# Performance work log

Measured on AMD Instinct MI355X. Metric: run time of the kernel, lower is better.

Reference implementation:

```python
import jax, jax.numpy as jnp
import numpy as np

D_MODEL = 256
NUM_WAVES = 8192
NUM_TRANSITIONS = 8192
NUM_TARGETS = 4096
BATCH = 4
TOP_K = 3


def setup_inputs() -> dict:
    key = jax.random.key(0)
    ks = jax.random.split(key, 16)
    d = D_MODEL
    inp = {
        'wave': jax.random.normal(ks[0], (BATCH, NUM_WAVES, d), jnp.float32),
        'transition': jax.random.normal(ks[1], (BATCH, NUM_TRANSITIONS, d), jnp.float32),
        'target': jax.random.normal(ks[2], (BATCH, NUM_TARGETS, d), jnp.float32),
        # learned adjacency logits (init: randn * 0.1)
        'w2t_adj': jax.random.normal(ks[3], (NUM_WAVES, NUM_TRANSITIONS), jnp.float32) * 0.1,
        't2t_adj': jax.random.normal(ks[4], (NUM_TRANSITIONS, NUM_TARGETS), jnp.float32) * 0.1,
        'temperature': jnp.array(1.0, jnp.float32),
        # gumbel noise (fixed sample, as drawn inside F.gumbel_softmax)
        'g_wt': jax.random.gumbel(ks[5], (NUM_WAVES, NUM_TRANSITIONS), jnp.float32),
        'g_tt': jax.random.gumbel(ks[6], (NUM_TRANSITIONS, NUM_TARGETS), jnp.float32),
        # wave->transition edge-weight predictor MLP: Linear(2d,d) ReLU Linear(d,1) Sigmoid
        'wt_w1': jax.random.normal(ks[7], (2 * d, d), jnp.float32) / np.sqrt(2 * d),
        'wt_b1': jnp.zeros((d,), jnp.float32),
        'wt_w2': jax.random.normal(ks[8], (d, 1), jnp.float32) / np.sqrt(d),
        'wt_b2': jnp.zeros((1,), jnp.float32),
        # transition->target predictor MLP
        'tt_w1': jax.random.normal(ks[9], (2 * d, d), jnp.float32) / np.sqrt(2 * d),
        'tt_b1': jnp.zeros((d,), jnp.float32),
        'tt_w2': jax.random.normal(ks[10], (d, 1), jnp.float32) / np.sqrt(d),
        'tt_b2': jnp.zeros((1,), jnp.float32),
    }
    return inp


def _gumbel_softmax(logits, gumbel_noise, tau):
    return jax.nn.softmax((logits + gumbel_noise) / tau, axis=-1)


def _generate_edges(probs, src_feat, tgt_feat, w1, b1, w2, b2):
    # probs: [S, T]; src_feat: [B, S, d]; tgt_feat: [B, T, d]
    S = probs.shape[0]
    top_vals, top_idx = jax.lax.top_k(probs, TOP_K)  # [S, k]
    src_idx = jnp.broadcast_to(jnp.arange(S)[:, None], (S, TOP_K)).reshape(-1)  # [S*k]
    tgt_idx = top_idx.reshape(-1)                                               # [S*k]
    edge_index = jnp.stack([src_idx, tgt_idx])                                  # [2, S*k]
    # gather node features of batch element 0 (as in the original code)
    e_src = src_feat[0][src_idx]                                                # [S*k, d]
    e_tgt = tgt_feat[0][tgt_idx]                                                # [S*k, d]
    e = jnp.concatenate([e_src, e_tgt], axis=-1)                                # [S*k, 2d]
    h = jax.nn.relu(e @ w1 + b1)
    mlp_w = jax.nn.sigmoid(h @ w2 + b2)[:, 0]                                   # [S*k]
    final_w = mlp_w * top_vals.reshape(-1)
    return edge_index, final_w


def reference(wave, transition, target, w2t_adj, t2t_adj, temperature,
              g_wt, g_tt, wt_w1, wt_b1, wt_w2, wt_b2,
              tt_w1, tt_b1, tt_w2, tt_b2):
    # training=True path: gumbel-softmax (soft) over adjacency logits
    wt_probs = _gumbel_softmax(w2t_adj, g_wt, temperature)
    tt_probs = _gumbel_softmax(t2t_adj, g_tt, temperature)
    wt_edges, wt_weights = _generate_edges(wt_probs, wave, transition,
                                           wt_w1, wt_b1, wt_w2, wt_b2)
    tt_edges, tt_weights = _generate_edges(tt_probs, transition, target,
                                           tt_w1, tt_b1, tt_w2, tt_b2)
    return wt_edges, wt_weights, tt_edges, tt_weights
```

## Files before the change

kernel.cpp:

```cpp
#include <hip/hip_runtime.h>

#define NWAVES 8192
#define NTRANS 8192
#define NTGT   4096
#define DMODEL 256
#define TOPK   3
#define EW (NWAVES * TOPK)
#define ET (NTRANS * TOPK)

struct TopkLds {
    float sv[256][3];
    int   si[256][3];
    float ss[256];
};
struct GemmLds {
    float As[32][68];
    float Bs[32][64];
};

template<int NCOLS>
__device__ __forceinline__ void topk_body(void* ldsraw, int row,
        const float* __restrict__ adj, const float* __restrict__ gum,
        float inv_tau,
        float* __restrict__ out_src, float* __restrict__ out_tgt,
        int* __restrict__ ws_idx, float* __restrict__ ws_val)
{
    TopkLds& L = *reinterpret_cast<TopkLds*>(ldsraw);
    const int tid = threadIdx.x;
    const float* ar = adj + (size_t)row * NCOLS;
    const float* gr = gum + (size_t)row * NCOLS;

    float v0 = -1e30f, v1 = -1e30f, v2 = -1e30f;
    int   i0 = 0, i1 = 0, i2 = 0;
    float s0 = 0.f, s1 = 0.f, s2 = 0.f, s3 = 0.f;

    auto upd3 = [&](float z, int c) {
        const bool gt0 = z > v0, gt1 = z > v1, gt2 = z > v2;
        v2 = gt1 ? v1 : fmaxf(z, v2);  i2 = gt1 ? i1 : (gt2 ? c : i2);
        v1 = gt0 ? v0 : fmaxf(z, v1);  i1 = gt0 ? i0 : (gt1 ? c : i1);
        v0 = fmaxf(z, v0);             i0 = gt0 ? c  : i0;
    };

#pragma unroll
    for (int base = 0; base < NCOLS; base += 1024) {
        const int c0 = base + tid * 4;
        const float4 a4 = *reinterpret_cast<const float4*>(ar + c0);
        const float4 g4 = *reinterpret_cast<const float4*>(gr + c0);
        const float za = fmaf(a4.x + g4.x, inv_tau, -10.0f);
        const float zb = fmaf(a4.y + g4.y, inv_tau, -10.0f);
        const float zc = fmaf(a4.z + g4.z, inv_tau, -10.0f);
        const float zd = fmaf(a4.w + g4.w, inv_tau, -10.0f);
        s0 += __expf(za); s1 += __expf(zb); s2 += __expf(zc); s3 += __expf(zd);
        upd3(za, c0); upd3(zb, c0 + 1); upd3(zc, c0 + 2); upd3(zd, c0 + 3);
    }

    L.sv[tid][0] = v0; L.sv[tid][1] = v1; L.sv[tid][2] = v2;
    L.si[tid][0] = i0; L.si[tid][1] = i1; L.si[tid][2] = i2;
    L.ss[tid] = (s0 + s1) + (s2 + s3);
    __syncthreads();

    for (int stride = 128; stride >= 1; stride >>= 1) {
        if (tid < stride) {
            const int o = tid + stride;
            float av[3] = {L.sv[tid][0], L.sv[tid][1], L.sv[tid][2]};
            int   ai[3] = {L.si[tid][0], L.si[tid][1], L.si[tid][2]};
            float bv[3] = {L.sv[o][0], L.sv[o][1], L.sv[o][2]};
            int   bi[3] = {L.si[o][0], L.si[o][1], L.si[o][2]};
            float rv[3]; int ri[3];
            int pa = 0, pb = 0;
#pragma unroll
            for (int q = 0; q < 3; ++q) {
                bool takeA;
                if (pb >= 3) takeA = true;
                else takeA = (av[pa] > bv[pb]) || (av[pa] == bv[pb] && ai[pa] < bi[pb]);
                if (takeA) { rv[q] = av[pa]; ri[q] = ai[pa]; ++pa; }
                else       { rv[q] = bv[pb]; ri[q] = bi[pb]; ++pb; }
            }
            L.sv[tid][0] = rv[0]; L.sv[tid][1] = rv[1]; L.sv[tid][2] = rv[2];
            L.si[tid][0] = ri[0]; L.si[tid][1] = ri[1]; L.si[tid][2] = ri[2];
            L.ss[tid] += L.ss[o];
        }
        __syncthreads();
    }

    if (tid < TOPK) {
        const float S = L.ss[0];
        const float p = __expf(L.sv[0][tid]) / S;
        const int idx = L.si[0][tid];
        const size_t e = (size_t)row * TOPK + tid;
        out_src[e] = (float)row;
        out_tgt[e] = (float)idx;
        ws_idx[e] = idx;
        ws_val[e] = p;
    }
}

__device__ __forceinline__ void gemm_body(void* ldsraw,
        const float* __restrict__ A, const float* __restrict__ B,
        float* __restrict__ C, int m0, int n0)
{
    GemmLds& L = *reinterpret_cast<GemmLds*>(ldsraw);
    const int tid = threadIdx.x;
    const int tx = tid % 16, ty = tid / 16;
    const int lc = tid % 32;
    const int lr = tid / 32;
    const int bn = tid % 64;
    const int bk = tid / 64;
    float acc[4][4] = {};

    for (int k0 = 0; k0 < DMODEL; k0 += 32) {
#pragma unroll
        for (int i = 0; i < 8; ++i) {
            const int r = lr + i * 8;
            L.As[lc][r] = A[(size_t)(m0 + r) * DMODEL + k0 + lc];
        }
#pragma unroll
        for (int i = 0; i < 8; ++i) {
            const int kk = bk + i * 4;
            L.Bs[kk][bn] = B[(size_t)(k0 + kk) * DMODEL + n0 + bn];
        }
        __syncthreads();
#pragma unroll
        for (int kk = 0; kk < 32; ++kk) {
            const float4 a4 = *reinterpret_cast<const float4*>(&L.As[kk][ty * 4]);
            const float4 b4 = *reinterpret_cast<const float4*>(&L.Bs[kk][tx * 4]);
            const float av[4] = {a4.x, a4.y, a4.z, a4.w};
            const float bv[4] = {b4.x, b4.y, b4.z, b4.w};
#pragma unroll
            for (int i = 0; i < 4; ++i)
#pragma unroll
                for (int j = 0; j < 4; ++j)
                    acc[i][j] += av[i] * bv[j];
        }
        __syncthreads();
    }
#pragma unroll
    for (int i = 0; i < 4; ++i) {
        float4 c4 = {acc[i][0], acc[i][1], acc[i][2], acc[i][3]};
        *reinterpret_cast<float4*>(&C[(size_t)(m0 + ty * 4 + i) * DMODEL + n0 + tx * 4]) = c4;
    }
}

__global__ __launch_bounds__(256)
void fused_main_kernel(const float* __restrict__ w2t, const float* __restrict__ g_wt,
                       const float* __restrict__ t2t, const float* __restrict__ g_tt,
                       const float* __restrict__ temp,
                       const float* __restrict__ wave, const float* __restrict__ trans,
                       const float* __restrict__ target,
                       const float* __restrict__ wt_w1, const float* __restrict__ tt_w1,
                       float* wt_src, float* wt_tgt, int* wt_idx, float* wt_val,
                       float* tt_src, float* tt_tgt, int* tt_idx, float* tt_val,
                       float* AW, float* BW, float* AT, float* BT,
                       int nGemm)
{
    __shared__ alignas(16) unsigned char ldsraw[sizeof(GemmLds)];
    const int bid = blockIdx.x;

    int topk_id, gemm_id = -1;
    if (nGemm > 0) {
        const int inter = nGemm * 10;
        if (bid < inter) {
            if (bid % 10 == 0) gemm_id = bid / 10;
            else topk_id = bid - bid / 10 - 1;
        } else {
            topk_id = bid - nGemm;
        }
    } else {
        topk_id = bid;
    }

    if (gemm_id >= 0) {
        const float* A; const float* B; float* C; int mblk, nblk;
        if (gemm_id < 512)       { A = wave;   B = wt_w1;                   C = AW; int g = gemm_id;        mblk = g % 128; nblk = g / 128; }
        else if (gemm_id < 1024) { A = trans;  B = wt_w1 + DMODEL * DMODEL; C = BW; int g = gemm_id - 512;  mblk = g % 128; nblk = g / 128; }
        else if (gemm_id < 1536) { A = trans;  B = tt_w1;                   C = AT; int g = gemm_id - 1024; mblk = g % 128; nblk = g / 128; }
        else                     { A = target; B = tt_w1 + DMODEL * DMODEL; C = BT; int g = gemm_id - 1536; mblk = g % 64;  nblk = g / 64;  }
        gemm_body(ldsraw, A, B, C, mblk * 64, nblk * 64);
        return;
    }

    const float inv_tau = 1.0f / temp[0];
    if (topk_id < NWAVES)
        topk_body<NTRANS>(ldsraw, topk_id, w2t, g_wt, inv_tau, wt_src, wt_tgt, wt_idx, wt_val);
    else
        topk_body<NTGT>(ldsraw, topk_id - NWAVES, t2t, g_tt, inv_tau, tt_src, tt_tgt, tt_idx, tt_val);
}

__global__ __launch_bounds__(256)
void edge_weight_fused_kernel(const float* __restrict__ AW, const float* __restrict__ BW,
                              const float* __restrict__ AT, const float* __restrict__ BT,
                              const int* __restrict__ wt_idx, const float* __restrict__ wt_val,
                              const int* __restrict__ tt_idx, const float* __restrict__ tt_val,
                              const float* __restrict__ wt_b1, const float* __restrict__ wt_w2, const float* __restrict__ wt_b2,
                              const float* __restrict__ tt_b1, const float* __restrict__ tt_w2, const float* __restrict__ tt_b2,
                              float* __restrict__ wt_out, float* __restrict__ tt_out)
{
    const int lane = threadIdx.x & 63;
    const int wv   = threadIdx.x >> 6;
    const int eg = blockIdx.x * 4 + wv;

    const bool isWT = (eg < EW);
    const int e = isWT ? eg : eg - EW;
    const float* Arows = isWT ? AW : AT;
    const float* Brows = isWT ? BW : BT;
    const int*   eidx  = isWT ? wt_idx : tt_idx;
    const float* evals = isWT ? wt_val : tt_val;
    const float* b1    = isWT ? wt_b1 : tt_b1;
    const float* w2    = isWT ? wt_w2 : tt_w2;
    const float* b2    = isWT ? wt_b2 : tt_b2;
    float*       outw  = isWT ? wt_out : tt_out;

    const int srow = e / 3;
    const int trow = eidx[e];
    const float4 a4 = *reinterpret_cast<const float4*>(Arows + (size_t)srow * DMODEL + lane * 4);
    const float4 b4 = *reinterpret_cast<const float4*>(Brows + (size_t)trow * DMODEL + lane * 4);
    const float4 c4 = *reinterpret_cast<const float4*>(b1 + lane * 4);
    const float4 w4 = *reinterpret_cast<const float4*>(w2 + lane * 4);
    float acc = fmaxf(a4.x + b4.x + c4.x, 0.f) * w4.x
              + fmaxf(a4.y + b4.y + c4.y, 0.f) * w4.y
              + fmaxf(a4.z + b4.z + c4.z, 0.f) * w4.z
              + fmaxf(a4.w + b4.w + c4.w, 0.f) * w4.w;
#pragma unroll
    for (int off = 32; off >= 1; off >>= 1) acc += __shfl_xor(acc, off);
    if (lane == 0) {
        const float x = acc + b2[0];
        const float sig = 1.0f / (1.0f + __expf(-x));
        outw[e] = sig * evals[e];
    }
}

__global__ __launch_bounds__(256)
void edge_mlp_direct_kernel(const float* __restrict__ src_feat,
                            const float* __restrict__ tgt_feat,
                            const int* __restrict__ eidx,
                            const float* __restrict__ evals,
                            const float* __restrict__ w1,
                            const float* __restrict__ b1,
                            const float* __restrict__ w2,
                            const float* __restrict__ b2,
                            float* __restrict__ out_w,
                            int nEdges)
{
    __shared__ float E[512][16];
    __shared__ float part[16][4];
    const int tid = threadIdx.x;
    const int e0 = blockIdx.x * 16;

    for (int i = tid; i < 16 * 128; i += 256) {
        const int e = i >> 7;
        const int q = i & 127;
        const int eg = e0 + e;
        float4 v;
        if (eg < nEdges) {
            if (q < 64) {
                const float* r = src_feat + (size_t)(eg / 3) * DMODEL;
                v = *reinterpret_cast<const float4*>(r + q * 4);
            } else {
                const float* r = tgt_feat + (size_t)eidx[eg] * DMODEL;
                v = *reinterpret_cast<const float4*>(r + (q - 64) * 4);
            }
        } else {
            v = make_float4(0.f, 0.f, 0.f, 0.f);
        }
        const int k = q * 4;
        E[k + 0][e] = v.x; E[k + 1][e] = v.y; E[k + 2][e] = v.z; E[k + 3][e] = v.w;
    }
    __syncthreads();

    const int j = tid;
    float acc[16];
#pragma unroll
    for (int e = 0; e < 16; ++e) acc[e] = 0.f;

    for (int k = 0; k < 512; ++k) {
        const float w = w1[(size_t)k * DMODEL + j];
        const float4 a = *reinterpret_cast<const float4*>(&E[k][0]);
        const float4 b = *reinterpret_cast<const float4*>(&E[k][4]);
        const float4 c = *reinterpret_cast<const float4*>(&E[k][8]);
        const float4 d = *reinterpret_cast<const float4*>(&E[k][12]);
        acc[0] += a.x * w;  acc[1] += a.y * w;  acc[2] += a.z * w;  acc[3] += a.w * w;
        acc[4] += b.x * w;  acc[5] += b.y * w;  acc[6] += b.z * w;  acc[7] += b.w * w;
        acc[8] += c.x * w;  acc[9] += c.y * w;  acc[10] += c.z * w; acc[11] += c.w * w;
        acc[12] += d.x * w; acc[13] += d.y * w; acc[14] += d.z * w; acc[15] += d.w * w;
    }

    const float b1j = b1[j];
    const float w2j = w2[j];
    const int lane = tid & 63;
    const int wv = tid >> 6;
#pragma unroll
    for (int e = 0; e < 16; ++e) {
        float v = fmaxf(acc[e] + b1j, 0.f) * w2j;
#pragma unroll
        for (int off = 32; off >= 1; off >>= 1) v += __shfl_xor(v, off);
        if (lane == 0) part[e][wv] = v;
    }
    __syncthreads();
    if (tid < 16) {
        const int eg = e0 + tid;
        if (eg < nEdges) {
            const float x = part[tid][0] + part[tid][1] + part[tid][2] + part[tid][3] + b2[0];
            const float sig = 1.0f / (1.0f + __expf(-x));
            out_w[eg] = sig * evals[eg];
        }
    }
}

extern "C" void kernel_launch(void* const* d_in, const int* in_sizes, int n_in,
                              void* d_out, int out_size, void* d_ws, size_t ws_size,
                              hipStream_t stream)
{
    const float* wave   = (const float*)d_in[0];
    const float* trans  = (const float*)d_in[1];
    const float* target = (const float*)d_in[2];
    const float* w2t    = (const float*)d_in[3];
    const float* t2t    = (const float*)d_in[4];
    const float* temp   = (const float*)d_in[5];
    const float* g_wt   = (const float*)d_in[6];
    const float* g_tt   = (const float*)d_in[7];
    const float* wt_w1  = (const float*)d_in[8];
    const float* wt_b1  = (const float*)d_in[9];
    const float* wt_w2  = (const float*)d_in[10];
    const float* wt_b2  = (const float*)d_in[11];
    const float* tt_w1  = (const float*)d_in[12];
    const float* tt_b1  = (const float*)d_in[13];
    const float* tt_w2  = (const float*)d_in[14];
    const float* tt_b2  = (const float*)d_in[15];

    float* out = (float*)d_out;
    float* wt_src = out;
    float* wt_tgt = out + EW;
    float* wt_wgt = out + 2 * EW;
    float* tt_src = out + 3 * EW;
    float* tt_tgt = out + 3 * EW + ET;
    float* tt_wgt = out + 3 * EW + 2 * ET;

    const size_t nodeFloats = (size_t)(NWAVES + NTRANS + NTRANS + NTGT) * DMODEL;
    const size_t edgeFloats = (size_t)(EW + ET);
    const size_t needBig = (nodeFloats + 2 * edgeFloats) * sizeof(float) + 2 * edgeFloats * sizeof(int);
    const bool bigPath = (ws_size >= needBig);

    float *AW = nullptr, *BW = nullptr, *AT = nullptr, *BT = nullptr;
    float *wt_val, *tt_val; int *wt_idx, *tt_idx;
    if (bigPath) {
        AW = (float*)d_ws;
        BW = AW + NWAVES * DMODEL;
        AT = BW + NTRANS * DMODEL;
        BT = AT + NTRANS * DMODEL;
        wt_val = BT + NTGT * DMODEL;
        tt_val = wt_val + EW;
        wt_idx = (int*)(tt_val + ET);
        tt_idx = wt_idx + EW;
    } else {
        wt_val = (float*)d_ws;
        tt_val = wt_val + EW;
        wt_idx = (int*)(tt_val + ET);
        tt_idx = wt_idx + EW;
    }

    const int nTopk = NWAVES + NTRANS;
    const int nGemm = bigPath ? (512 * 3 + 256) : 0;
    const int grid = nTopk + nGemm;

    fused_main_kernel<<<grid, 256, 0, stream>>>(
        w2t, g_wt, t2t, g_tt, temp, wave, trans, target, wt_w1, tt_w1,
        wt_src, wt_tgt, wt_idx, wt_val, tt_src, tt_tgt, tt_idx, tt_val,
        AW, BW, AT, BT, nGemm);

    if (bigPath) {
        edge_weight_fused_kernel<<<(EW + ET) / 4, 256, 0, stream>>>(
            AW, BW, AT, BT, wt_idx, wt_val, tt_idx, tt_val,
            wt_b1, wt_w2, wt_b2, tt_b1, tt_w2, tt_b2, wt_wgt, tt_wgt);
    } else {
        edge_mlp_direct_kernel<<<(EW + 15) / 16, 256, 0, stream>>>(wave,  trans,  wt_idx, wt_val, wt_w1, wt_b1, wt_w2, wt_b2, wt_wgt, EW);
        edge_mlp_direct_kernel<<<(ET + 15) / 16, 256, 0, stream>>>(trans, target, tt_idx, tt_val, tt_w1, tt_b1, tt_w2, tt_b2, tt_wgt, ET);
    }
}
```

Measured before the change: 216.2 us.

## Process one top-k row per wavefront with shuffle reduction and prefetching

Each top-k row is now handled by a single 64-lane wavefront instead of a whole 256-thread block, and the LDS tree reduction with its many __syncthreads is replaced by xor-shuffle merges of the per-lane top-3. Each lane keeps two interleaved top-3 lists, using med3 for the inserts, and software-prefetches four float4s ahead. The GEMM/top-k block interleave ratio changes to match the 4x smaller top-k block count. The goal is to remove barrier and LDS overhead and raise memory-level parallelism in this bandwidth-bound scan. In exchange each lane now scans 4x more columns and holds more registers.

Result: faster. 204.2 us (-5.6%).

```diff
diff --git a/kernel.cpp b/kernel.cpp
--- a/kernel.cpp
+++ b/kernel.cpp
@@ -8,90 +8,102 @@
 #define EW (NWAVES * TOPK)
 #define ET (NTRANS * TOPK)
 
-struct TopkLds {
-    float sv[256][3];
-    int   si[256][3];
-    float ss[256];
-};
 struct GemmLds {
     float As[32][68];
     float Bs[32][64];
 };
 
 template<int NCOLS>
-__device__ __forceinline__ void topk_body(void* ldsraw, int row,
-        const float* __restrict__ adj, const float* __restrict__ gum,
-        float inv_tau,
+__device__ __forceinline__ void topk_wave_body(int row, int lane,
+        const float* __restrict__ adj, const float* __restrict__ gum, float inv_tau,
         float* __restrict__ out_src, float* __restrict__ out_tgt,
         int* __restrict__ ws_idx, float* __restrict__ ws_val)
 {
-    TopkLds& L = *reinterpret_cast<TopkLds*>(ldsraw);
-    const int tid = threadIdx.x;
-    const float* ar = adj + (size_t)row * NCOLS;
-    const float* gr = gum + (size_t)row * NCOLS;
-
-    float v0 = -1e30f, v1 = -1e30f, v2 = -1e30f;
-    int   i0 = 0, i1 = 0, i2 = 0;
+    constexpr int NIT = NCOLS / 256;
+    const float4* ap = reinterpret_cast<const float4*>(adj + (size_t)row * NCOLS) + lane;
+    const float4* gp = reinterpret_cast<const float4*>(gum + (size_t)row * NCOLS) + lane;
+    const int lane4 = lane * 4;
+
+    float av0 = -1e30f, av1 = -1e30f, av2 = -1e30f; int ai0 = 0, ai1 = 0, ai2 = 0;
+    float bv0 = -1e30f, bv1 = -1e30f, bv2 = -1e30f; int bi0 = 0, bi1 = 0, bi2 = 0;
     float s0 = 0.f, s1 = 0.f, s2 = 0.f, s3 = 0.f;
 
-    auto upd3 = [&](float z, int c) {
-        const bool gt0 = z > v0, gt1 = z > v1, gt2 = z > v2;
-        v2 = gt1 ? v1 : fmaxf(z, v2);  i2 = gt1 ? i1 : (gt2 ? c : i2);
-        v1 = gt0 ? v0 : fmaxf(z, v1);  i1 = gt0 ? i0 : (gt1 ? c : i1);
-        v0 = fmaxf(z, v0);             i0 = gt0 ? c  : i0;
+    auto insA = [&](float z, int c) {
+        const bool g0 = z > av0, g1 = z > av1, g2 = z > av2;
+        av2 = __builtin_amdgcn_fmed3f(z, av1, av2);
+        ai2 = g1 ? ai1 : (g2 ? c : ai2);
+        av1 = __builtin_amdgcn_fmed3f(z, av0, av1);
+        ai1 = g0 ? ai0 : (g1 ? c : ai1);
+        av0 = fmaxf(z, av0);
+        ai0 = g0 ? c : ai0;
     };
-
-#pragma unroll
-    for (int base = 0; base < NCOLS; base += 1024) {
-        const int c0 = base + tid * 4;
-        const float4 a4 = *reinterpret_cast<const float4*>(ar + c0);
-        const float4 g4 = *reinterpret_cast<const float4*>(gr + c0);
-        const float za = fmaf(a4.x + g4.x, inv_tau, -10.0f);
-        const float zb = fmaf(a4.y + g4.y, inv_tau, -10.0f);
-        const float zc = fmaf(a4.z + g4.z, inv_tau, -10.0f);
-        const float zd = fmaf(a4.w + g4.w, inv_tau, -10.0f);
+    auto insB = [&](float z, int c) {
+        const bool g0 = z > bv0, g1 = z > bv1, g2 = z > bv2;
+        bv2 = __builtin_amdgcn_fmed3f(z, bv1, bv2);
+        bi2 = g1 ? bi1 : (g2 ? c : bi2);
+        bv1 = __builtin_amdgcn_fmed3f(z, bv0, bv1);
+        bi1 = g0 ? bi0 : (g1 ? c : bi1);
+        bv0 = fmaxf(z, bv0);
+        bi0 = g0 ? c : bi0;
+    };
+    auto proc = [&](const float4& a, const float4& g, int it) {
+        const int cb = it * 256 + lane4;
+        const float za = fmaf(a.x + g.x, inv_tau, -10.0f);
+        const float zb = fmaf(a.y + g.y, inv_tau, -10.0f);
+        const float zc = fmaf(a.z + g.z, inv_tau, -10.0f);
+        const float zd = fmaf(a.w + g.w, inv_tau, -10.0f);
         s0 += __expf(za); s1 += __expf(zb); s2 += __expf(zc); s3 += __expf(zd);
-        upd3(za, c0); upd3(zb, c0 + 1); upd3(zc, c0 + 2); upd3(zd, c0 + 3);
-    }
-
-    L.sv[tid][0] = v0; L.sv[tid][1] = v1; L.sv[tid][2] = v2;
-    L.si[tid][0] = i0; L.si[tid][1] = i1; L.si[tid][2] = i2;
-    L.ss[tid] = (s0 + s1) + (s2 + s3);
-    __syncthreads();
-
-    for (int stride = 128; stride >= 1; stride >>= 1) {
-        if (tid < stride) {
-            const int o = tid + stride;
-            float av[3] = {L.sv[tid][0], L.sv[tid][1], L.sv[tid][2]};
-            int   ai[3] = {L.si[tid][0], L.si[tid][1], L.si[tid][2]};
-            float bv[3] = {L.sv[o][0], L.sv[o][1], L.sv[o][2]};
-            int   bi[3] = {L.si[o][0], L.si[o][1], L.si[o][2]};
-            float rv[3]; int ri[3];
-            int pa = 0, pb = 0;
-#pragma unroll
-            for (int q = 0; q < 3; ++q) {
-                bool takeA;
-                if (pb >= 3) takeA = true;
-                else takeA = (av[pa] > bv[pb]) || (av[pa] == bv[pb] && ai[pa] < bi[pb]);
-                if (takeA) { rv[q] = av[pa]; ri[q] = ai[pa]; ++pa; }
-                else       { rv[q] = bv[pb]; ri[q] = bi[pb]; ++pb; }
-            }
-            L.sv[tid][0] = rv[0]; L.sv[tid][1] = rv[1]; L.sv[tid][2] = rv[2];
-            L.si[tid][0] = ri[0]; L.si[tid][1] = ri[1]; L.si[tid][2] = ri[2];
-            L.ss[tid] += L.ss[o];
-        }
-        __syncthreads();
-    }
-
-    if (tid < TOPK) {
-        const float S = L.ss[0];
-        const float p = __expf(L.sv[0][tid]) / S;
-        const int idx = L.si[0][tid];
-        const size_t e = (size_t)row * TOPK + tid;
-        out_src[e] = (float)row;
-        out_tgt[e] = (float)idx;
-        ws_idx[e] = idx;
-        ws_val[e] = p;
+        insA(za, cb); insA(zb, cb | 1); insB(zc, cb | 2); insB(zd, cb | 3);
+    };
+
+    float4 A0 = ap[0 * 64], A1 = ap[1 * 64], A2 = ap[2 * 64], A3 = ap[3 * 64];
+    float4 G0 = gp[0 * 64], G1 = gp[1 * 64], G2 = gp[2 * 64], G3 = gp[3 * 64];
+#pragma unroll
+    for (int it = 0; it < NIT; it += 4) {
+        const bool more = (it + 4) < NIT;
+        proc(A0, G0, it + 0);
+        if (more) { A0 = ap[(it + 4) * 64]; G0 = gp[(it + 4) * 64]; }
+        proc(A1, G1, it + 1);
+        if (more) { A1 = ap[(it + 5) * 64]; G1 = gp[(it + 5) * 64]; }
+        proc(A2, G2, it + 2);
+        if (more) { A2 = ap[(it + 6) * 64]; G2 = gp[(it + 6) * 64]; }
+        proc(A3, G3, it + 3);
+        if (more) { A3 = ap[(it + 7) * 64]; G3 = gp[(it + 7) * 64]; }
+    }
+
+    auto insIA = [&](float z, int c) {
+        const bool e0 = (z == av0), e1 = (z == av1), e2 = (z == av2);
+        const bool g0 = (z > av0) || (e0 && c < ai0);
+        const bool g1 = (z > av1) || (e1 && c < ai1);
+        const bool g2 = (z > av2) || (e2 && c < ai2);
+        av2 = __builtin_amdgcn_fmed3f(z, av1, av2);
+        ai2 = g1 ? ai1 : (g2 ? c : ai2);
+        av1 = __builtin_amdgcn_fmed3f(z, av0, av1);
+        ai1 = g0 ? ai0 : (g1 ? c : ai1);
+        av0 = fmaxf(z, av0);
+        ai0 = g0 ? c : ai0;
+    };
+
+    insIA(bv0, bi0); insIA(bv1, bi1); insIA(bv2, bi2);
+    float s = (s0 + s1) + (s2 + s3);
+
+#pragma unroll
+    for (int m = 1; m < 64; m <<= 1) {
+        const float u0 = __shfl_xor(av0, m), u1 = __shfl_xor(av1, m), u2 = __shfl_xor(av2, m);
+        const int   j0 = __shfl_xor(ai0, m), j1 = __shfl_xor(ai1, m), j2 = __shfl_xor(ai2, m);
+        s += __shfl_xor(s, m);
+        insIA(u0, j0); insIA(u1, j1); insIA(u2, j2);
+    }
+
+    if (lane == 0) {
+        const float invS = 1.0f / s;
+        const size_t e = (size_t)row * TOPK;
+        out_src[e] = (float)row; out_src[e + 1] = (float)row; out_src[e + 2] = (float)row;
+        out_tgt[e] = (float)ai0; out_tgt[e + 1] = (float)ai1; out_tgt[e + 2] = (float)ai2;
+        ws_idx[e] = ai0; ws_idx[e + 1] = ai1; ws_idx[e + 2] = ai2;
+        ws_val[e] = __expf(av0) * invS;
+        ws_val[e + 1] = __expf(av1) * invS;
+        ws_val[e + 2] = __expf(av2) * invS;
     }
 }
 
@@ -156,12 +168,12 @@
     __shared__ alignas(16) unsigned char ldsraw[sizeof(GemmLds)];
     const int bid = blockIdx.x;
 
-    int topk_id, gemm_id = -1;
+    int topk_id = -1, gemm_id = -1;
     if (nGemm > 0) {
-        const int inter = nGemm * 10;
+        const int inter = nGemm * 3;
         if (bid < inter) {
-            if (bid % 10 == 0) gemm_id = bid / 10;
-            else topk_id = bid - bid / 10 - 1;
+            if (bid % 3 == 0) gemm_id = bid / 3;
+            else topk_id = bid - bid / 3 - 1;
         } else {
             topk_id = bid - nGemm;
         }
@@ -171,19 +183,22 @@
 
     if (gemm_id >= 0) {
         const float* A; const float* B; float* C; int mblk, nblk;
-        if (gemm_id < 512)       { A = wave;   B = wt_w1;                   C = AW; int g = gemm_id;        mblk = g % 128; nblk = g / 128; }
-        else if (gemm_id < 1024) { A = trans;  B = wt_w1 + DMODEL * DMODEL; C = BW; int g = gemm_id - 512;  mblk = g % 128; nblk = g / 128; }
-        else if (gemm_id < 1536) { A = trans;  B = tt_w1;                   C = AT; int g = gemm_id - 1024; mblk = g % 128; nblk = g / 128; }
-        else                     { A = target; B = tt_w1 + DMODEL * DMODEL; C = BT; int g = gemm_id - 1536; mblk = g % 64;  nblk = g / 64;  }
+        if (gemm_id < 512)       { A = wave;   B = wt_w1;                    C = AW; int g = gemm_id;        mblk = g % 128; nblk = g / 128; }
+        else if (gemm_id < 1024) { A = trans;  B = wt_w1 + DMODEL * DMODEL;  C = BW; int g = gemm_id - 512;  mblk = g % 128; nblk = g / 128; }
+        else if (gemm_id < 1536) { A = trans;  B = tt_w1;                    C = AT; int g = gemm_id - 1024; mblk = g % 128; nblk = g / 128; }
+        else                     { A = target; B = tt_w1 + DMODEL * DMODEL;  C = BT; int g = gemm_id - 1536; mblk = g % 64;  nblk = g / 64;  }
         gemm_body(ldsraw, A, B, C, mblk * 64, nblk * 64);
         return;
     }
 
+    const int lane = threadIdx.x & 63;
+    const int wv = threadIdx.x >> 6;
+    const int row = topk_id * 4 + wv;
     const float inv_tau = 1.0f / temp[0];
-    if (topk_id < NWAVES)
-        topk_body<NTRANS>(ldsraw, topk_id, w2t, g_wt, inv_tau, wt_src, wt_tgt, wt_idx, wt_val);
+    if (row < NWAVES)
+        topk_wave_body<NTRANS>(row, lane, w2t, g_wt, inv_tau, wt_src, wt_tgt, wt_idx, wt_val);
     else
-        topk_body<NTGT>(ldsraw, topk_id - NWAVES, t2t, g_tt, inv_tau, tt_src, tt_tgt, tt_idx, tt_val);
+        topk_wave_body<NTGT>(row - NWAVES, lane, t2t, g_tt, inv_tau, tt_src, tt_tgt, tt_idx, tt_val);
 }
 
 __global__ __launch_bounds__(256)
@@ -358,9 +373,9 @@
         tt_idx = wt_idx + EW;
     }
 
-    const int nTopk = NWAVES + NTRANS;
+    const int nTopkBlocks = (NWAVES + NTRANS) / 4;
     const int nGemm = bigPath ? (512 * 3 + 256) : 0;
-    const int grid = nTopk + nGemm;
+    const int grid = nTopkBlocks + nGemm;
 
     fused_main_kernel<<<grid, 256, 0, stream>>>(
         w2t, g_wt, t2t, g_tt, temp, wave, trans, target, wt_w1, tt_w1,
```
